# Kernel optimization log

Measured on AMD Instinct MI355X. Metric: run time of the kernel, lower is better.

The kernel has to match this reference:

```python
import jax, jax.numpy as jnp
import numpy as np

B, T, I, H = 128, 1024, 256, 512


def setup_inputs() -> dict:
    key = jax.random.key(0)
    k_x, k_wih, k_whh, k_bih, k_bhh = jax.random.split(key, 5)
    s = 1.0 / np.sqrt(H)  # PyTorch LSTMCell init scale
    x = jax.random.normal(k_x, (B, T, I), dtype=jnp.float32)
    W_ih = jax.random.uniform(k_wih, (4 * H, I), minval=-s, maxval=s, dtype=jnp.float32)
    W_hh = jax.random.uniform(k_whh, (4 * H, H), minval=-s, maxval=s, dtype=jnp.float32)
    b_ih = jax.random.uniform(k_bih, (4 * H,), minval=-s, maxval=s, dtype=jnp.float32)
    b_hh = jax.random.uniform(k_bhh, (4 * H,), minval=-s, maxval=s, dtype=jnp.float32)
    return {"x": x, "W_ih": W_ih, "W_hh": W_hh, "b_ih": b_ih, "b_hh": b_hh}


def _lstm_final_h(x, W_ih, W_hh, b_ih, b_hh):
    Bn, Tn, _ = x.shape
    Hn = W_hh.shape[1]
    # Precompute input-side gate projections for all timesteps: [T, B, 4H]
    x_gates = jnp.einsum('bti,gi->tbg', x, W_ih) + b_ih + b_hh

    def step(carry, xg_t):
        h, c = carry
        gates = xg_t + h @ W_hh.T  # [B, 4H]
        i_g, f_g, g_g, o_g = jnp.split(gates, 4, axis=-1)
        i_g = jax.nn.sigmoid(i_g)
        f_g = jax.nn.sigmoid(f_g)
        g_g = jnp.tanh(g_g)
        o_g = jax.nn.sigmoid(o_g)
        c = f_g * c + i_g * g_g
        h = o_g * jnp.tanh(c)
        return (h, c), None

    h0 = jnp.zeros((Bn, Hn), dtype=x.dtype)
    c0 = jnp.zeros((Bn, Hn), dtype=x.dtype)
    (h_T, _), _ = jax.lax.scan(step, (h0, c0), x_gates)
    return h_T


def reference(x, W_ih, W_hh, b_ih, b_hh):
    # Module returns only the final hidden state h_t (outputs list is unused,
    # self.out and dropout are never applied).
    return _lstm_final_h(x, W_ih, W_hh, b_ih, b_hh)
```

## Files before the change

### kernel.cpp

```cpp
#include <hip/hip_runtime.h>
#include <stdint.h>


#define Bsz 128
#define Tsz 1024
#define Isz 256
#define Hsz 512
#define NBLK 128
#define NTHREADS 512

typedef __attribute__((ext_vector_type(8))) short short8;
typedef __attribute__((ext_vector_type(4))) float float4v;
typedef __attribute__((ext_vector_type(4))) unsigned int uint4v;
typedef __attribute__((ext_vector_type(2))) unsigned int uint2v;

__device__ __forceinline__ float b2f(unsigned short u) {
  union { float f; unsigned int i; } v; v.i = ((unsigned int)u) << 16; return v.f;
}
__device__ __forceinline__ unsigned short f2b(float f) {
  unsigned int u = __float_as_uint(f);
  return (unsigned short)((u + 0x7fffu + ((u >> 16) & 1u)) >> 16);
}
__device__ __forceinline__ float sigmf(float x) { return 1.0f / (1.0f + __expf(-x)); }
__device__ __forceinline__ float tanhf_fast(float x) {
  float e = __expf(-2.0f * fabsf(x));
  float t = (1.0f - e) / (1.0f + e);
  return copysignf(t, x);
}
__device__ __forceinline__ short8 cvt8r(float4v u, float4v v) {
  short8 r;
  r[0] = (short)f2b(u[0]); r[1] = (short)f2b(u[1]);
  r[2] = (short)f2b(u[2]); r[3] = (short)f2b(u[3]);
  r[4] = (short)f2b(v[0]); r[5] = (short)f2b(v[1]);
  r[6] = (short)f2b(v[2]); r[7] = (short)f2b(v[3]);
  return r;
}

#define MFMA(A, B, C) __builtin_amdgcn_mfma_f32_16x16x32_bf16((A), (B), (C), 0, 0, 0)

#define LLD(dst, base, OFFB)                                              \
  asm volatile("global_load_dwordx4 %0, %1, off offset:" OFFB " sc0 sc1"  \
               : "=v"(dst) : "v"(base))
#define XLD(dst, base, OFFB)                                              \
  asm volatile("global_load_dwordx4 %0, %1, off offset:" OFFB             \
               : "=v"(dst) : "v"(base))
#define VMW(N)                                                            \
  do { asm volatile("s_waitcnt vmcnt(" #N ")" ::: "memory");              \
       __builtin_amdgcn_sched_barrier(0); } while (0)

__global__ __launch_bounds__(NTHREADS, 2) void lstm_persistent(
    const float* __restrict__ x,
    const float* __restrict__ wih,
    const float* __restrict__ whh,
    const float* __restrict__ bih,
    const float* __restrict__ bhh,
    float* __restrict__ out,
    unsigned int* __restrict__ hb0,
    unsigned int* __restrict__ hb1,
    unsigned int* __restrict__ flags)
{
  __shared__ short8 hhi_pl[1024];
  __shared__ short8 hlo_pl[1024];
  __shared__ short8 x_pl[2][512];

  const int tid  = threadIdx.x;
  const int wid  = tid >> 6;
  const int lane = tid & 63;
  const int l15  = lane & 15;
  const int kq   = lane >> 4;
  const int qg   = l15 >> 2;
  const int ug   = l15 & 3;
  const int blk  = blockIdx.x;
  const int dom  = blk >> 4;
  const int bi   = blk & 15;
  const int col  = qg * Hsz + bi * 32 + wid * 4 + ug;
  const int rowbase = dom * 16;

  short8 wx[8], whhhi[16], whhlo[16];
  {
    const float* p = wih + (size_t)col * Isz + kq * 8;
#pragma unroll
    for (int ks = 0; ks < 8; ++ks) {
      float4v u0 = *(const float4v*)(p + ks * 32);
      float4v u1 = *(const float4v*)(p + ks * 32 + 4);
      wx[ks] = cvt8r(u0, u1);
    }
  }
  {
    const float* p = whh + (size_t)col * Hsz + kq * 8;
#pragma unroll
    for (int ks = 0; ks < 16; ++ks) {
      float4v u0 = *(const float4v*)(p + ks * 32);
      float4v u1 = *(const float4v*)(p + ks * 32 + 4);
      short8 hi = cvt8r(u0, u1);
      short8 lo;
#pragma unroll
      for (int e = 0; e < 4; ++e) {
        lo[e]     = (short)f2b(u0[e] - b2f((unsigned short)hi[e]));
        lo[e + 4] = (short)f2b(u1[e] - b2f((unsigned short)hi[e + 4]));
      }
      whhhi[ks] = hi; whhlo[ks] = lo;
    }
  }
  const float biasC = bih[col] + bhh[col];

  unsigned int* myf = flags + dom * 1024 + bi * 64 + wid;
  const unsigned int* pollp = flags + dom * 1024 + (lane >> 2) * 64 + (lane & 3) * 2;

  const int srow = tid & 15;
  const int grow = rowbase + srow;
  const int cidx = tid >> 4;
  const int f1   = (cidx >> 1) * 64 + (cidx & 1) * 32 + srow;
  const float* xsrc0 = x + (size_t)grow * (Tsz * Isz) + cidx * 8;

  {
    float4v u0, u1;
    XLD(u0, xsrc0, "0"); XLD(u1, xsrc0, "16");
    VMW(0);
    x_pl[0][tid] = cvt8r(u0, u1);
  }
  __syncthreads();

  float cstv = 0.f;
  const int growo = rowbase + kq * 4 + qg;
  const int hunit = bi * 32 + wid * 4 + ug;

  for (int t = 0; t < Tsz; ++t) {
    const int par = t & 1;

    float4v xu0, xu1;
    const int tn = (t + 1 < Tsz) ? t + 1 : t;
    {
      const float* xp = xsrc0 + (size_t)tn * Isz;
      XLD(xu0, xp, "0"); XLD(xu1, xp, "16");
    }

    float4v accm = {0.f, 0.f, 0.f, 0.f};
    float4v accc = {0.f, 0.f, 0.f, 0.f};
#pragma unroll
    for (int ks = 0; ks < 8; ++ks) {
      short8 xa = x_pl[par][ks * 64 + lane];
      accm = MFMA(xa, wx[ks], accm);
    }

    if (t > 0 && wid == 0) {
      int guard = 0;
      for (;;) {
        uint2v fv;
        asm volatile("global_load_dwordx2 %0, %1, off sc0 sc1\n\t"
                     "s_waitcnt vmcnt(0)"
                     : "=v"(fv) : "v"(pollp) : "memory");
        unsigned m = fv[0] < fv[1] ? fv[0] : fv[1];
        if (__all(m >= (unsigned)t)) break;
        __builtin_amdgcn_s_sleep(1);
        if (++guard > (1 << 26)) break;
      }
    }
    __syncthreads();

    const unsigned int* hsrc =
        ((par) ? hb1 : hb0) + (size_t)grow * Hsz + cidx * 16;
    uint4v d0, d1, d2, d3;
    LLD(d0, hsrc, "0");  LLD(d1, hsrc, "16");
    LLD(d2, hsrc, "32"); LLD(d3, hsrc, "48");

    VMW(4);
    if (t + 1 < Tsz)
      x_pl[par ^ 1][tid] = cvt8r(xu0, xu1);

    VMW(0);
    {
      short8 h0, h1, l0, l1;
#pragma unroll
      for (int e = 0; e < 4; ++e) {
        h0[e]     = (short)(d0[e] & 0xffffu); l0[e]     = (short)(d0[e] >> 16);
        h0[e + 4] = (short)(d1[e] & 0xffffu); l0[e + 4] = (short)(d1[e] >> 16);
        h1[e]     = (short)(d2[e] & 0xffffu); l1[e]     = (short)(d2[e] >> 16);
        h1[e + 4] = (short)(d3[e] & 0xffffu); l1[e + 4] = (short)(d3[e] >> 16);
      }
      hhi_pl[f1]      = h0;  hlo_pl[f1]      = l0;
      hhi_pl[f1 + 16] = h1;  hlo_pl[f1 + 16] = l1;
    }
    __syncthreads();

#pragma unroll
    for (int ks = 0; ks < 16; ++ks) {
      short8 ha = hhi_pl[ks * 64 + lane];
      short8 la = hlo_pl[ks * 64 + lane];
      accm = MFMA(ha, whhhi[ks], accm);
      accc = MFMA(ha, whhlo[ks], accc);
      accc = MFMA(la, whhhi[ks], accc);
    }

    float v0 = accm[0] + accc[0] + biasC;
    float v1 = accm[1] + accc[1] + biasC;
    float v2 = accm[2] + accc[2] + biasC;
    float v3 = accm[3] + accc[3] + biasC;
    int k1 = qg ^ 1, k2 = qg ^ 2, k3 = qg ^ 3;
    float s0 = (qg == 0) ? v0 : (qg == 1) ? v1 : (qg == 2) ? v2 : v3;
    float s1 = (k1 == 0) ? v0 : (k1 == 1) ? v1 : (k1 == 2) ? v2 : v3;
    float s2 = (k2 == 0) ? v0 : (k2 == 1) ? v1 : (k2 == 2) ? v2 : v3;
    float s3 = (k3 == 0) ? v0 : (k3 == 1) ? v1 : (k3 == 2) ? v2 : v3;
    float r4  = __shfl_xor(s1, 4, 64);
    float r8  = __shfl_xor(s2, 8, 64);
    float r12 = __shfl_xor(s3, 12, 64);
    float gi = (qg == 0) ? s0 : (qg == 1) ? r4 : (qg == 2) ? r8 : r12;
    float gf = (qg == 1) ? s0 : (qg == 0) ? r4 : (qg == 3) ? r8 : r12;
    float gG = (qg == 2) ? s0 : (qg == 3) ? r4 : (qg == 0) ? r8 : r12;
    float go = (qg == 3) ? s0 : (qg == 2) ? r4 : (qg == 1) ? r8 : r12;

    float ig = sigmf(gi);
    float fg = sigmf(gf);
    float gg = tanhf_fast(gG);
    float og = sigmf(go);
    float c  = fg * cstv + ig * gg;
    cstv = c;
    float hv = og * tanhf_fast(c);

    if (t == Tsz - 1) {
      out[(size_t)growo * Hsz + hunit] = hv;
    } else {
      unsigned short hi16 = f2b(hv);
      unsigned short lo16 = f2b(hv - b2f(hi16));
      unsigned int pk = (unsigned int)hi16 | ((unsigned int)lo16 << 16);
      unsigned int* pp = ((par) ? hb0 : hb1) + (size_t)growo * Hsz + hunit;
      asm volatile("global_store_dword %0, %1, off sc0 sc1"
                   :: "v"(pp), "v"(pk) : "memory");
      asm volatile("s_waitcnt vmcnt(0)" ::: "memory");
      if (lane == 0) {
        unsigned int fv = (unsigned)(t + 1);
        asm volatile("global_store_dword %0, %1, off sc0 sc1"
                     :: "v"(myf), "v"(fv) : "memory");
      }
    }
  }
}

extern "C" void kernel_launch(void* const* d_in, const int* in_sizes, int n_in,
                              void* d_out, int out_size, void* d_ws, size_t ws_size,
                              hipStream_t stream) {
  if (n_in < 5) return;
  long long s0 = in_sizes[0], s1 = in_sizes[1], s2 = in_sizes[2],
            s3 = in_sizes[3], s4 = in_sizes[4];
  if (!(s1 > 0 && s3 > 0 && s0 == 64 * s1 && s2 == 2 * s1 &&
        s1 == 256 * s3 && s3 == s4)) return;

  const float* x   = (const float*)d_in[0];
  const float* wih = (const float*)d_in[1];
  const float* whh = (const float*)d_in[2];
  const float* bih = (const float*)d_in[3];
  const float* bhh = (const float*)d_in[4];
  float* out = (float*)d_out;

  char* ws = (char*)d_ws;
  const size_t FLAGS_BYTES = 8 * 4096;
  const size_t HB = (size_t)Bsz * Hsz * 4;
  unsigned int* flags = (unsigned int*)ws;
  unsigned int* hb0 = (unsigned int*)(ws + FLAGS_BYTES);
  unsigned int* hb1 = (unsigned int*)(ws + FLAGS_BYTES + HB);

  hipMemsetAsync(d_ws, 0, FLAGS_BYTES + 2 * HB, stream);

  hipLaunchKernelGGL(lstm_persistent, dim3(NBLK), dim3(NTHREADS), 0, stream,
                     x, wih, whh, bih, bhh, out, hb0, hb1, flags);
}
```

Baseline: 5.080 ms.

## Split LSTM across 256 blocks of 4 waves and defer flag publish

```diff
diff --git a/kernel.cpp b/kernel.cpp
--- a/kernel.cpp
+++ b/kernel.cpp
@@ -6,8 +6,8 @@
 #define Tsz 1024
 #define Isz 256
 #define Hsz 512
-#define NBLK 128
-#define NTHREADS 512
+#define NBLK 256
+#define NTHREADS 256
 
 typedef __attribute__((ext_vector_type(8))) short short8;
 typedef __attribute__((ext_vector_type(4))) float float4v;
@@ -34,6 +34,19 @@
   r[4] = (short)f2b(v[0]); r[5] = (short)f2b(v[1]);
   r[6] = (short)f2b(v[2]); r[7] = (short)f2b(v[3]);
   return r;
+}
+__device__ __forceinline__ unsigned int cvtpk(float a, float b) {
+  unsigned int r;
+  asm("v_cvt_pk_bf16_f32 %0, %1, %2" : "=v"(r) : "v"(a), "v"(b));
+  return r;
+}
+__device__ __forceinline__ short8 cvt8pk(float4v u, float4v v) {
+  union { unsigned int d[4]; short8 s; } r;
+  r.d[0] = cvtpk(u[0], u[1]);
+  r.d[1] = cvtpk(u[2], u[3]);
+  r.d[2] = cvtpk(v[0], v[1]);
+  r.d[3] = cvtpk(v[2], v[3]);
+  return r.s;
 }
 
 #define MFMA(A, B, C) __builtin_amdgcn_mfma_f32_16x16x32_bf16((A), (B), (C), 0, 0, 0)
@@ -48,7 +61,21 @@
   do { asm volatile("s_waitcnt vmcnt(" #N ")" ::: "memory");              \
        __builtin_amdgcn_sched_barrier(0); } while (0)
 
-__global__ __launch_bounds__(NTHREADS, 2) void lstm_persistent(
+#define UNPACK_Q(q, dA, dB) do {                                          \
+    short8 h8, l8;                                                        \
+    h8[0]=(short)(dA[0]&0xffffu); l8[0]=(short)(dA[0]>>16);               \
+    h8[1]=(short)(dA[1]&0xffffu); l8[1]=(short)(dA[1]>>16);               \
+    h8[2]=(short)(dA[2]&0xffffu); l8[2]=(short)(dA[2]>>16);               \
+    h8[3]=(short)(dA[3]&0xffffu); l8[3]=(short)(dA[3]>>16);               \
+    h8[4]=(short)(dB[0]&0xffffu); l8[4]=(short)(dB[0]>>16);               \
+    h8[5]=(short)(dB[1]&0xffffu); l8[5]=(short)(dB[1]>>16);               \
+    h8[6]=(short)(dB[2]&0xffffu); l8[6]=(short)(dB[2]>>16);               \
+    h8[7]=(short)(dB[3]&0xffffu); l8[7]=(short)(dB[3]>>16);               \
+    hhi_pl[fh + (q) * 16] = h8;                                           \
+    hlo_pl[fh + (q) * 16] = l8;                                           \
+  } while (0)
+
+__global__ __launch_bounds__(NTHREADS, 1) void lstm_persistent(
     const float* __restrict__ x,
     const float* __restrict__ wih,
     const float* __restrict__ whh,
@@ -71,9 +98,9 @@
   const int qg   = l15 >> 2;
   const int ug   = l15 & 3;
   const int blk  = blockIdx.x;
-  const int dom  = blk >> 4;
-  const int bi   = blk & 15;
-  const int col  = qg * Hsz + bi * 32 + wid * 4 + ug;
+  const int dom  = blk >> 5;
+  const int bi   = blk & 31;
+  const int col  = qg * Hsz + bi * 16 + wid * 4 + ug;
   const int rowbase = dom * 16;
 
   short8 wx[8], whhhi[16], whhlo[16];
@@ -104,98 +131,109 @@
   }
   const float biasC = bih[col] + bhh[col];
 
-  unsigned int* myf = flags + dom * 1024 + bi * 64 + wid;
-  const unsigned int* pollp = flags + dom * 1024 + (lane >> 2) * 64 + (lane & 3) * 2;
+  unsigned int* myf = flags + dom * 2048 + bi * 64 + wid;
+  const unsigned int* pollp = flags + dom * 2048 + (lane >> 1) * 64 + (lane & 1) * 2;
 
   const int srow = tid & 15;
   const int grow = rowbase + srow;
   const int cidx = tid >> 4;
-  const int f1   = (cidx >> 1) * 64 + (cidx & 1) * 32 + srow;
-  const float* xsrc0 = x + (size_t)grow * (Tsz * Isz) + cidx * 8;
+  const int fh   = cidx * 64 + srow;
+  const int fx   = (cidx >> 1) * 64 + (cidx & 1) * 32 + srow;
+  const float* xsrc0 = x + (size_t)grow * (Tsz * Isz) + cidx * 16;
 
   {
-    float4v u0, u1;
-    XLD(u0, xsrc0, "0"); XLD(u1, xsrc0, "16");
+    float4v u0, u1, u2, u3;
+    XLD(u0, xsrc0, "0");  XLD(u1, xsrc0, "16");
+    XLD(u2, xsrc0, "32"); XLD(u3, xsrc0, "48");
     VMW(0);
-    x_pl[0][tid] = cvt8r(u0, u1);
+    x_pl[0][fx]      = cvt8pk(u0, u1);
+    x_pl[0][fx + 16] = cvt8pk(u2, u3);
   }
   __syncthreads();
 
   float cstv = 0.f;
   const int growo = rowbase + kq * 4 + qg;
-  const int hunit = bi * 32 + wid * 4 + ug;
+  const int hunit = bi * 16 + wid * 4 + ug;
 
   for (int t = 0; t < Tsz; ++t) {
     const int par = t & 1;
 
-    float4v xu0, xu1;
+    float4v xu0, xu1, xu2, xu3;
     const int tn = (t + 1 < Tsz) ? t + 1 : t;
     {
       const float* xp = xsrc0 + (size_t)tn * Isz;
-      XLD(xu0, xp, "0"); XLD(xu1, xp, "16");
-    }
-
-    float4v accm = {0.f, 0.f, 0.f, 0.f};
-    float4v accc = {0.f, 0.f, 0.f, 0.f};
-#pragma unroll
-    for (int ks = 0; ks < 8; ++ks) {
-      short8 xa = x_pl[par][ks * 64 + lane];
-      accm = MFMA(xa, wx[ks], accm);
-    }
-
-    if (t > 0 && wid == 0) {
-      int guard = 0;
-      for (;;) {
-        uint2v fv;
-        asm volatile("global_load_dwordx2 %0, %1, off sc0 sc1\n\t"
-                     "s_waitcnt vmcnt(0)"
-                     : "=v"(fv) : "v"(pollp) : "memory");
-        unsigned m = fv[0] < fv[1] ? fv[0] : fv[1];
-        if (__all(m >= (unsigned)t)) break;
-        __builtin_amdgcn_s_sleep(1);
-        if (++guard > (1 << 26)) break;
+      XLD(xu0, xp, "0");  XLD(xu1, xp, "16");
+      XLD(xu2, xp, "32"); XLD(xu3, xp, "48");
+    }
+
+    float4v accm  = {0.f, 0.f, 0.f, 0.f};
+    float4v accc1 = {0.f, 0.f, 0.f, 0.f};
+    float4v accc2 = {0.f, 0.f, 0.f, 0.f};
+#pragma unroll
+    for (int ks = 0; ks < 8; ks += 2) {
+      short8 xa0 = x_pl[par][ks * 64 + lane];
+      short8 xa1 = x_pl[par][(ks + 1) * 64 + lane];
+      accm  = MFMA(xa0, wx[ks], accm);
+      accc1 = MFMA(xa1, wx[ks + 1], accc1);
+    }
+
+    if (t > 0) {
+      VMW(4);
+      if (lane == 0) {
+        unsigned int fv = (unsigned)t;
+        asm volatile("global_store_dword %0, %1, off sc0 sc1"
+                     :: "v"(myf), "v"(fv) : "memory");
       }
+      if (wid == 0) {
+        int guard = 0;
+        for (;;) {
+          uint2v fv;
+          asm volatile("global_load_dwordx2 %0, %1, off sc0 sc1\n\t"
+                       "s_waitcnt vmcnt(0)"
+                       : "=v"(fv) : "v"(pollp) : "memory");
+          unsigned m = fv[0] < fv[1] ? fv[0] : fv[1];
+          if (__all(m >= (unsigned)t)) break;
+          __builtin_amdgcn_s_sleep(1);
+          if (++guard > (1 << 22)) break;
+        }
+      }
     }
     __syncthreads();
 
     const unsigned int* hsrc =
-        ((par) ? hb1 : hb0) + (size_t)grow * Hsz + cidx * 16;
-    uint4v d0, d1, d2, d3;
+        (par ? hb1 : hb0) + (size_t)grow * Hsz + cidx * 32;
+    uint4v d0, d1, d2, d3, d4, d5, d6, d7;
     LLD(d0, hsrc, "0");  LLD(d1, hsrc, "16");
     LLD(d2, hsrc, "32"); LLD(d3, hsrc, "48");
-
-    VMW(4);
-    if (t + 1 < Tsz)
-      x_pl[par ^ 1][tid] = cvt8r(xu0, xu1);
+    LLD(d4, hsrc, "64"); LLD(d5, hsrc, "80");
+    LLD(d6, hsrc, "96"); LLD(d7, hsrc, "112");
+
+    VMW(8);
+    if (t + 1 < Tsz) {
+      x_pl[par ^ 1][fx]      = cvt8pk(xu0, xu1);
+      x_pl[par ^ 1][fx + 16] = cvt8pk(xu2, xu3);
+    }
 
     VMW(0);
-    {
-      short8 h0, h1, l0, l1;
-#pragma unroll
-      for (int e = 0; e < 4; ++e) {
-        h0[e]     = (short)(d0[e] & 0xffffu); l0[e]     = (short)(d0[e] >> 16);
-        h0[e + 4] = (short)(d1[e] & 0xffffu); l0[e + 4] = (short)(d1[e] >> 16);
-        h1[e]     = (short)(d2[e] & 0xffffu); l1[e]     = (short)(d2[e] >> 16);
-        h1[e + 4] = (short)(d3[e] & 0xffffu); l1[e + 4] = (short)(d3[e] >> 16);
-      }
-      hhi_pl[f1]      = h0;  hlo_pl[f1]      = l0;
-      hhi_pl[f1 + 16] = h1;  hlo_pl[f1 + 16] = l1;
-    }
+    UNPACK_Q(0, d0, d1);
+    UNPACK_Q(1, d2, d3);
+    UNPACK_Q(2, d4, d5);
+    UNPACK_Q(3, d6, d7);
     __syncthreads();
 
 #pragma unroll
     for (int ks = 0; ks < 16; ++ks) {
       short8 ha = hhi_pl[ks * 64 + lane];
       short8 la = hlo_pl[ks * 64 + lane];
-      accm = MFMA(ha, whhhi[ks], accm);
-      accc = MFMA(ha, whhlo[ks], accc);
-      accc = MFMA(la, whhhi[ks], accc);
-    }
-
-    float v0 = accm[0] + accc[0] + biasC;
-    float v1 = accm[1] + accc[1] + biasC;
-    float v2 = accm[2] + accc[2] + biasC;
-    float v3 = accm[3] + accc[3] + biasC;
+      accm  = MFMA(ha, whhhi[ks], accm);
+      accc1 = MFMA(ha, whhlo[ks], accc1);
+      accc2 = MFMA(la, whhhi[ks], accc2);
+    }
+
+    float v0 = (accm[0] + accc1[0]) + accc2[0] + biasC;
+    float v1 = (accm[1] + accc1[1]) + accc2[1] + biasC;
+    float v2 = (accm[2] + accc1[2]) + accc2[2] + biasC;
+    float v3 = (accm[3] + accc1[3]) + accc2[3] + biasC;
     int k1 = qg ^ 1, k2 = qg ^ 2, k3 = qg ^ 3;
     float s0 = (qg == 0) ? v0 : (qg == 1) ? v1 : (qg == 2) ? v2 : v3;
     float s1 = (k1 == 0) ? v0 : (k1 == 1) ? v1 : (k1 == 2) ? v2 : v3;
@@ -223,15 +261,9 @@
       unsigned short hi16 = f2b(hv);
       unsigned short lo16 = f2b(hv - b2f(hi16));
       unsigned int pk = (unsigned int)hi16 | ((unsigned int)lo16 << 16);
-      unsigned int* pp = ((par) ? hb0 : hb1) + (size_t)growo * Hsz + hunit;
+      unsigned int* pp = (par ? hb0 : hb1) + (size_t)growo * Hsz + hunit;
       asm volatile("global_store_dword %0, %1, off sc0 sc1"
                    :: "v"(pp), "v"(pk) : "memory");
-      asm volatile("s_waitcnt vmcnt(0)" ::: "memory");
-      if (lane == 0) {
-        unsigned int fv = (unsigned)(t + 1);
-        asm volatile("global_store_dword %0, %1, off sc0 sc1"
-                     :: "v"(myf), "v"(fv) : "memory");
-      }
     }
   }
 }
@@ -253,7 +285,7 @@
   float* out = (float*)d_out;
 
   char* ws = (char*)d_ws;
-  const size_t FLAGS_BYTES = 8 * 4096;
+  const size_t FLAGS_BYTES = 8 * 2048 * 4;
   const size_t HB = (size_t)Bsz * Hsz * 4;
   unsigned int* flags = (unsigned int*)ws;
   unsigned int* hb0 = (unsigned int*)(ws + FLAGS_BYTES);
```

After: 5.527 ms. 1.09x slower.

## Replace flag-based step sync with parity tags embedded in hidden-state data

Applied to the files above, without the earlier changes.

```diff
diff --git a/kernel.cpp b/kernel.cpp
--- a/kernel.cpp
+++ b/kernel.cpp
@@ -12,7 +12,6 @@
 typedef __attribute__((ext_vector_type(8))) short short8;
 typedef __attribute__((ext_vector_type(4))) float float4v;
 typedef __attribute__((ext_vector_type(4))) unsigned int uint4v;
-typedef __attribute__((ext_vector_type(2))) unsigned int uint2v;
 
 __device__ __forceinline__ float b2f(unsigned short u) {
   union { float f; unsigned int i; } v; v.i = ((unsigned int)u) << 16; return v.f;
@@ -34,6 +33,19 @@
   r[4] = (short)f2b(v[0]); r[5] = (short)f2b(v[1]);
   r[6] = (short)f2b(v[2]); r[7] = (short)f2b(v[3]);
   return r;
+}
+__device__ __forceinline__ unsigned int cvtpk(float a, float b) {
+  unsigned int r;
+  asm("v_cvt_pk_bf16_f32 %0, %1, %2" : "=v"(r) : "v"(a), "v"(b));
+  return r;
+}
+__device__ __forceinline__ short8 cvt8pk(float4v u, float4v v) {
+  union { unsigned int d[4]; short8 s; } r;
+  r.d[0] = cvtpk(u[0], u[1]);
+  r.d[1] = cvtpk(u[2], u[3]);
+  r.d[2] = cvtpk(v[0], v[1]);
+  r.d[3] = cvtpk(v[2], v[3]);
+  return r.s;
 }
 
 #define MFMA(A, B, C) __builtin_amdgcn_mfma_f32_16x16x32_bf16((A), (B), (C), 0, 0, 0)
@@ -56,11 +68,10 @@
     const float* __restrict__ bhh,
     float* __restrict__ out,
     unsigned int* __restrict__ hb0,
-    unsigned int* __restrict__ hb1,
-    unsigned int* __restrict__ flags)
+    unsigned int* __restrict__ hb1)
 {
-  __shared__ short8 hhi_pl[1024];
-  __shared__ short8 hlo_pl[1024];
+  __shared__ short8 hhi_pl[2][1024];
+  __shared__ short8 hlo_pl[2][1024];
   __shared__ short8 x_pl[2][512];
 
   const int tid  = threadIdx.x;
@@ -104,9 +115,6 @@
   }
   const float biasC = bih[col] + bhh[col];
 
-  unsigned int* myf = flags + dom * 1024 + bi * 64 + wid;
-  const unsigned int* pollp = flags + dom * 1024 + (lane >> 2) * 64 + (lane & 3) * 2;
-
   const int srow = tid & 15;
   const int grow = rowbase + srow;
   const int cidx = tid >> 4;
@@ -117,7 +125,7 @@
     float4v u0, u1;
     XLD(u0, xsrc0, "0"); XLD(u1, xsrc0, "16");
     VMW(0);
-    x_pl[0][tid] = cvt8r(u0, u1);
+    x_pl[0][tid] = cvt8pk(u0, u1);
   }
   __syncthreads();
 
@@ -143,32 +151,28 @@
       accm = MFMA(xa, wx[ks], accm);
     }
 
-    if (t > 0 && wid == 0) {
+    const unsigned int* hsrc =
+        (par ? hb1 : hb0) + (size_t)grow * Hsz + cidx * 16;
+    const unsigned int tagm = ((unsigned int)((t >> 1) & 1)) << 16;
+    uint4v d0, d1, d2, d3;
+    {
       int guard = 0;
       for (;;) {
-        uint2v fv;
-        asm volatile("global_load_dwordx2 %0, %1, off sc0 sc1\n\t"
-                     "s_waitcnt vmcnt(0)"
-                     : "=v"(fv) : "v"(pollp) : "memory");
-        unsigned m = fv[0] < fv[1] ? fv[0] : fv[1];
-        if (__all(m >= (unsigned)t)) break;
+        LLD(d0, hsrc, "0");  LLD(d1, hsrc, "16");
+        LLD(d2, hsrc, "32"); LLD(d3, hsrc, "48");
+        VMW(0);
+        unsigned int a =
+            (d0[0] ^ tagm) | (d0[1] ^ tagm) | (d0[2] ^ tagm) | (d0[3] ^ tagm) |
+            (d1[0] ^ tagm) | (d1[1] ^ tagm) | (d1[2] ^ tagm) | (d1[3] ^ tagm) |
+            (d2[0] ^ tagm) | (d2[1] ^ tagm) | (d2[2] ^ tagm) | (d2[3] ^ tagm) |
+            (d3[0] ^ tagm) | (d3[1] ^ tagm) | (d3[2] ^ tagm) | (d3[3] ^ tagm);
+        if (!(a & 0x00010000u)) break;
         __builtin_amdgcn_s_sleep(1);
-        if (++guard > (1 << 26)) break;
+        if (++guard > (1 << 20)) break;
       }
     }
-    __syncthreads();
-
-    const unsigned int* hsrc =
-        ((par) ? hb1 : hb0) + (size_t)grow * Hsz + cidx * 16;
-    uint4v d0, d1, d2, d3;
-    LLD(d0, hsrc, "0");  LLD(d1, hsrc, "16");
-    LLD(d2, hsrc, "32"); LLD(d3, hsrc, "48");
-
-    VMW(4);
-    if (t + 1 < Tsz)
-      x_pl[par ^ 1][tid] = cvt8r(xu0, xu1);
-
-    VMW(0);
+
+    if (t + 1 < Tsz) x_pl[par ^ 1][tid] = cvt8pk(xu0, xu1);
     {
       short8 h0, h1, l0, l1;
 #pragma unroll
@@ -178,15 +182,15 @@
         h1[e]     = (short)(d2[e] & 0xffffu); l1[e]     = (short)(d2[e] >> 16);
         h1[e + 4] = (short)(d3[e] & 0xffffu); l1[e + 4] = (short)(d3[e] >> 16);
       }
-      hhi_pl[f1]      = h0;  hlo_pl[f1]      = l0;
-      hhi_pl[f1 + 16] = h1;  hlo_pl[f1 + 16] = l1;
+      hhi_pl[par][f1]      = h0;  hlo_pl[par][f1]      = l0;
+      hhi_pl[par][f1 + 16] = h1;  hlo_pl[par][f1 + 16] = l1;
     }
     __syncthreads();
 
 #pragma unroll
     for (int ks = 0; ks < 16; ++ks) {
-      short8 ha = hhi_pl[ks * 64 + lane];
-      short8 la = hlo_pl[ks * 64 + lane];
+      short8 ha = hhi_pl[par][ks * 64 + lane];
+      short8 la = hlo_pl[par][ks * 64 + lane];
       accm = MFMA(ha, whhhi[ks], accm);
       accc = MFMA(ha, whhlo[ks], accc);
       accc = MFMA(la, whhhi[ks], accc);
@@ -222,16 +226,12 @@
     } else {
       unsigned short hi16 = f2b(hv);
       unsigned short lo16 = f2b(hv - b2f(hi16));
+      lo16 = (unsigned short)((lo16 & 0xFFFEu) |
+                              ((unsigned int)((t + 1) >> 1) & 1u));
       unsigned int pk = (unsigned int)hi16 | ((unsigned int)lo16 << 16);
-      unsigned int* pp = ((par) ? hb0 : hb1) + (size_t)growo * Hsz + hunit;
+      unsigned int* pp = (par ? hb0 : hb1) + (size_t)growo * Hsz + hunit;
       asm volatile("global_store_dword %0, %1, off sc0 sc1"
                    :: "v"(pp), "v"(pk) : "memory");
-      asm volatile("s_waitcnt vmcnt(0)" ::: "memory");
-      if (lane == 0) {
-        unsigned int fv = (unsigned)(t + 1);
-        asm volatile("global_store_dword %0, %1, off sc0 sc1"
-                     :: "v"(myf), "v"(fv) : "memory");
-      }
     }
   }
 }
@@ -253,14 +253,13 @@
   float* out = (float*)d_out;
 
   char* ws = (char*)d_ws;
-  const size_t FLAGS_BYTES = 8 * 4096;
   const size_t HB = (size_t)Bsz * Hsz * 4;
-  unsigned int* flags = (unsigned int*)ws;
-  unsigned int* hb0 = (unsigned int*)(ws + FLAGS_BYTES);
-  unsigned int* hb1 = (unsigned int*)(ws + FLAGS_BYTES + HB);
-
-  hipMemsetAsync(d_ws, 0, FLAGS_BYTES + 2 * HB, stream);
+  unsigned int* hb0 = (unsigned int*)ws;
+  unsigned int* hb1 = (unsigned int*)(ws + HB);
+
+  hipMemsetAsync(hb0, 0x00, HB, stream);
+  hipMemsetAsync(hb1, 0x01, HB, stream);
 
   hipLaunchKernelGGL(lstm_persistent, dim3(NBLK), dim3(NTHREADS), 0, stream,
-                     x, wih, whh, bih, bhh, out, hb0, hb1, flags);
-}
+                     x, wih, whh, bih, bhh, out, hb0, hb1);
+}
```

Result: slower. 5.324 ms (+4.8%).
